# Kernel tuning notes

Hardware: AMD Instinct MI355X
Metric: run time of the kernel (lower is better)

The kernel has to match this reference:

```python
import jax, jax.numpy as jnp
import numpy as np

B, N, F, R, DEG, STEPS = 4, 1024, 128, 16, 16, 2


def setup_inputs() -> dict:
    key = jax.random.key(0)
    ks = jax.random.split(key, 12)
    BN = B * N
    E = BN * DEG

    def edges(k):
        # edges kept within each graph of size N, then offset per graph
        e = jax.random.randint(k, (2, E), 0, N)
        off = jnp.repeat(jnp.arange(B, dtype=jnp.int32) * N, N * DEG)
        return e + off[None, :]

    return {
        "x_s": jax.random.normal(ks[0], (BN, F), jnp.float32),
        "edge_index_s": edges(ks[1]),
        "x_t": jax.random.normal(ks[2], (BN, F), jnp.float32),
        "edge_index_t": edges(ks[3]),
        "W1_self": jax.random.normal(ks[4], (F, F), jnp.float32) / np.float32(np.sqrt(F)),
        "W1_nbr": jax.random.normal(ks[5], (F, F), jnp.float32) / np.float32(np.sqrt(F)),
        "b1": jnp.zeros((F,), jnp.float32),
        "W2_self": jax.random.normal(ks[6], (R, R), jnp.float32) / np.float32(np.sqrt(R)),
        "W2_nbr": jax.random.normal(ks[7], (R, R), jnp.float32) / np.float32(np.sqrt(R)),
        "b2": jnp.zeros((R,), jnp.float32),
        "Wm1": jax.random.normal(ks[8], (R, R), jnp.float32) / np.float32(np.sqrt(R)),
        "bm1": jnp.zeros((R,), jnp.float32),
        "Wm2": jax.random.normal(ks[9], (R, 1), jnp.float32) / np.float32(np.sqrt(R)),
        "bm2": jnp.zeros((1,), jnp.float32),
        "r_steps": jax.random.normal(ks[10], (STEPS, B, N, R), jnp.float32),
    }


def _psi(x, ei, Ws, Wn, b):
    # simple GraphConv: self transform + summed neighbor transform
    agg = jax.ops.segment_sum(x[ei[0]], ei[1], num_segments=x.shape[0])
    return jax.nn.relu(x @ Ws + agg @ Wn + b)


def reference(x_s, edge_index_s, x_t, edge_index_t, W1_self, W1_nbr, b1,
              W2_self, W2_nbr, b2, Wm1, bm1, Wm2, bm2, r_steps):
    # psi_1 on both graphs, then dense-batch to [B, N, F] (equal-size graphs,
    # so masks are all-True and masked_softmax == softmax)
    h_s = _psi(x_s, edge_index_s, W1_self, W1_nbr, b1).reshape(B, N, F)
    h_t = _psi(x_t, edge_index_t, W1_self, W1_nbr, b1).reshape(B, N, F)

    S_hat = jnp.einsum('bsf,btf->bst', h_s, h_t)  # [B, Ns, Nt]
    S_0 = jax.nn.softmax(S_hat, axis=-1)

    for i in range(STEPS):
        S = jax.nn.softmax(S_hat, axis=-1)
        r_s = r_steps[i]                             # [B, N, R]
        r_t = jnp.einsum('bst,bsr->btr', S, r_s)     # S^T @ r_s
        o_s = _psi(r_s.reshape(B * N, R), edge_index_s, W2_self, W2_nbr, b2).reshape(B, N, R)
        o_t = _psi(r_t.reshape(B * N, R), edge_index_t, W2_self, W2_nbr, b2).reshape(B, N, R)
        D = o_s[:, :, None, :] - o_t[:, None, :, :]  # [B, Ns, Nt, R]
        upd = (jax.nn.relu(D @ Wm1 + bm1) @ Wm2 + bm2)[..., 0]
        S_hat = S_hat + upd

    S_L = jax.nn.softmax(S_hat, axis=-1)
    return (S_0, S_L)
```

## Files before the change

### kernel.cpp

```cpp
#include <hip/hip_runtime.h>

#define B_ 4
#define N_ 1024
#define F_ 128
#define R_ 16
#define E_ 65536
#define BN_ 4096

__global__ __launch_bounds__(256) void hist_k(
    const int* __restrict__ eis, const int* __restrict__ eit, int* __restrict__ counts) {
  const int* ei = blockIdx.y ? eit : eis;
  int* c = counts + blockIdx.y * BN_;
  int e = blockIdx.x * 256 + threadIdx.x;
  atomicAdd(c + ei[E_ + e], 1);
}

__global__ __launch_bounds__(256) void csr_scan(
    const int* __restrict__ counts, int* __restrict__ offs, int* __restrict__ cursor) {
  const int* c = counts + blockIdx.x * BN_;
  int* o = offs + blockIdx.x * (BN_ + 1);
  int* cur = cursor + blockIdx.x * BN_;
  int tid = threadIdx.x;
  int base = tid * 16;
  int local[16], sum = 0;
#pragma unroll
  for (int i = 0; i < 16; i++) { local[i] = sum; sum += c[base + i]; }
  __shared__ int csum[256];
  csum[tid] = sum;
  __syncthreads();
  for (int d = 1; d < 256; d <<= 1) {
    int v = (tid >= d) ? csum[tid - d] : 0;
    __syncthreads();
    csum[tid] += v;
    __syncthreads();
  }
  int prev = (tid == 0) ? 0 : csum[tid - 1];
#pragma unroll
  for (int i = 0; i < 16; i++) { int off = prev + local[i]; o[base + i] = off; cur[base + i] = off; }
  if (tid == 255) o[BN_] = csum[255];
}

__global__ __launch_bounds__(256) void csr_fill(
    const int* __restrict__ eis, const int* __restrict__ eit,
    int* __restrict__ cursor, int* __restrict__ csr) {
  const int* ei = blockIdx.y ? eit : eis;
  int* cur = cursor + blockIdx.y * BN_;
  int* cs = csr + blockIdx.y * E_;
  int e = blockIdx.x * 256 + threadIdx.x;
  int src = ei[e], dst = ei[E_ + e];
  int pos = atomicAdd(cur + dst, 1);
  cs[pos] = src;
}

__global__ __launch_bounds__(256) void gather_f(
    const float* __restrict__ xs, const float* __restrict__ xt,
    const int* __restrict__ csr, const int* __restrict__ offs,
    float* __restrict__ aggs, float* __restrict__ aggt) {
  const float* x = blockIdx.y ? xt : xs;
  const int* cs = csr + blockIdx.y * E_;
  const int* of = offs + blockIdx.y * (BN_ + 1);
  float* agg = blockIdx.y ? aggt : aggs;
  int node = blockIdx.x * 2 + (threadIdx.x >> 7);
  int ch = threadIdx.x & 127;
  int j0 = of[node], j1 = of[node + 1];
  float a0 = 0.f, a1 = 0.f, a2 = 0.f, a3 = 0.f;
  int j = j0;
  for (; j + 3 < j1; j += 4) {
    int s0 = cs[j], s1 = cs[j + 1], s2 = cs[j + 2], s3 = cs[j + 3];
    a0 += x[(size_t)s0 * F_ + ch];
    a1 += x[(size_t)s1 * F_ + ch];
    a2 += x[(size_t)s2 * F_ + ch];
    a3 += x[(size_t)s3 * F_ + ch];
  }
  for (; j < j1; j++) a0 += x[(size_t)cs[j] * F_ + ch];
  agg[(size_t)node * F_ + ch] = (a0 + a1) + (a2 + a3);
}

__global__ __launch_bounds__(256) void psi1_gemm(
    const float* __restrict__ xs, const float* __restrict__ aggs,
    const float* __restrict__ xt, const float* __restrict__ aggt,
    const float* __restrict__ Ws, const float* __restrict__ Wn,
    const float* __restrict__ bias, float* __restrict__ hs, float* __restrict__ ht) {
  const float* x   = blockIdx.z ? xt   : xs;
  const float* agg = blockIdx.z ? aggt : aggs;
  float*       h   = blockIdx.z ? ht   : hs;
  int n0 = blockIdx.x * 64, m0 = blockIdx.y * 64;
  int tid = threadIdx.x, tx = tid & 15, ty = tid >> 4;
  __shared__ __align__(16) float sA[16][68];
  __shared__ __align__(16) float sB[16][68];
  float acc[4][4] = {};
  for (int phase = 0; phase < 2; phase++) {
    const float* A  = phase ? agg : x;
    const float* Bw = phase ? Wn  : Ws;
    for (int kb = 0; kb < F_; kb += 16) {
      int row = tid >> 2, k4 = (tid & 3) * 4;
      float4 va = *(const float4*)(A + (size_t)(m0 + row) * F_ + kb + k4);
      sA[k4 + 0][row] = va.x; sA[k4 + 1][row] = va.y;
      sA[k4 + 2][row] = va.z; sA[k4 + 3][row] = va.w;
      int k = tid >> 4, n4 = (tid & 15) * 4;
      *(float4*)&sB[k][n4] = *(const float4*)(Bw + (size_t)(kb + k) * F_ + n0 + n4);
      __syncthreads();
#pragma unroll
      for (int kk = 0; kk < 16; kk++) {
        float a[4], bb[4];
        *(float4*)a  = *(const float4*)&sA[kk][ty * 4];
        *(float4*)bb = *(const float4*)&sB[kk][tx * 4];
#pragma unroll
        for (int i = 0; i < 4; i++)
#pragma unroll
          for (int j = 0; j < 4; j++) acc[i][j] += a[i] * bb[j];
      }
      __syncthreads();
    }
  }
  float4 bv = *(const float4*)(bias + n0 + tx * 4);
  float bj[4] = {bv.x, bv.y, bv.z, bv.w};
#pragma unroll
  for (int i = 0; i < 4; i++) {
    int m = m0 + ty * 4 + i;
    float4 o;
    o.x = fmaxf(acc[i][0] + bj[0], 0.f); o.y = fmaxf(acc[i][1] + bj[1], 0.f);
    o.z = fmaxf(acc[i][2] + bj[2], 0.f); o.w = fmaxf(acc[i][3] + bj[3], 0.f);
    *(float4*)(h + (size_t)m * F_ + n0 + tx * 4) = o;
  }
}

__global__ __launch_bounds__(256) void shat_gemm(
    const float* __restrict__ hs, const float* __restrict__ ht, float* __restrict__ S) {
  int b = blockIdx.z;
  int n0 = blockIdx.x * 128, m0 = blockIdx.y * 128;
  int tid = threadIdx.x, tx = tid & 15, ty = tid >> 4;
  __shared__ __align__(16) float sA[16][132];
  __shared__ __align__(16) float sB[16][132];
  float acc[8][8] = {};
  const float* Ag = hs + (size_t)(b * N_ + m0) * F_;
  const float* Bg = ht + (size_t)(b * N_ + n0) * F_;
  for (int kb = 0; kb < F_; kb += 16) {
#pragma unroll
    for (int l = 0; l < 2; l++) {
      int idx = tid + l * 256;
      int row = idx >> 2, k4 = (idx & 3) * 4;
      float4 va = *(const float4*)(Ag + (size_t)row * F_ + kb + k4);
      sA[k4 + 0][row] = va.x; sA[k4 + 1][row] = va.y;
      sA[k4 + 2][row] = va.z; sA[k4 + 3][row] = va.w;
      float4 vb = *(const float4*)(Bg + (size_t)row * F_ + kb + k4);
      sB[k4 + 0][row] = vb.x; sB[k4 + 1][row] = vb.y;
      sB[k4 + 2][row] = vb.z; sB[k4 + 3][row] = vb.w;
    }
    __syncthreads();
#pragma unroll
    for (int kk = 0; kk < 16; kk++) {
      float a[8], bb[8];
      *(float4*)&a[0]  = *(const float4*)&sA[kk][ty * 8];
      *(float4*)&a[4]  = *(const float4*)&sA[kk][ty * 8 + 4];
      *(float4*)&bb[0] = *(const float4*)&sB[kk][tx * 8];
      *(float4*)&bb[4] = *(const float4*)&sB[kk][tx * 8 + 4];
#pragma unroll
      for (int i = 0; i < 8; i++)
#pragma unroll
        for (int j = 0; j < 8; j++) acc[i][j] += a[i] * bb[j];
    }
    __syncthreads();
  }
#pragma unroll
  for (int i = 0; i < 8; i++) {
    size_t off = ((size_t)(b * N_ + m0 + ty * 8 + i)) * N_ + n0 + tx * 8;
    float4 o0 = {acc[i][0], acc[i][1], acc[i][2], acc[i][3]};
    float4 o1 = {acc[i][4], acc[i][5], acc[i][6], acc[i][7]};
    *(float4*)(S + off) = o0; *(float4*)(S + off + 4) = o1;
  }
}

__global__ __launch_bounds__(256) void softmax_row(
    const float* __restrict__ in, float* __restrict__ out) {
  int row = blockIdx.x;
  float4 v = ((const float4*)(in + (size_t)row * N_))[threadIdx.x];
  float m = fmaxf(fmaxf(v.x, v.y), fmaxf(v.z, v.w));
#pragma unroll
  for (int o = 32; o > 0; o >>= 1) m = fmaxf(m, __shfl_down(m, o, 64));
  __shared__ float rmax[4], rsum[4];
  int wave = threadIdx.x >> 6, lane = threadIdx.x & 63;
  if (lane == 0) rmax[wave] = m;
  __syncthreads();
  m = fmaxf(fmaxf(rmax[0], rmax[1]), fmaxf(rmax[2], rmax[3]));
  float e0 = __expf(v.x - m), e1 = __expf(v.y - m);
  float e2 = __expf(v.z - m), e3 = __expf(v.w - m);
  float s = e0 + e1 + e2 + e3;
#pragma unroll
  for (int o = 32; o > 0; o >>= 1) s += __shfl_down(s, o, 64);
  if (lane == 0) rsum[wave] = s;
  __syncthreads();
  s = rsum[0] + rsum[1] + rsum[2] + rsum[3];
  float inv = 1.f / s;
  float4 o4 = {e0 * inv, e1 * inv, e2 * inv, e3 * inv};
  ((float4*)(out + (size_t)row * N_))[threadIdx.x] = o4;
}

template <bool EXP>
__global__ __launch_bounds__(256) void rt_part_k(
    const float* __restrict__ S, const float2* __restrict__ stats,
    const float* __restrict__ rs, float* __restrict__ part) {
  int b = blockIdx.z, c = blockIdx.y, t0 = blockIdx.x * 256;
  int tid = threadIdx.x;
  int s0 = c * 32;
  __shared__ float rsh[32][16];
  __shared__ float sstat[64];
  if (tid < 128) {
    int srow = tid >> 2, c4 = (tid & 3) * 4;
    float4 v = *(const float4*)(rs + ((size_t)(b * N_ + s0 + srow)) * R_ + c4);
    rsh[srow][c4] = v.x; rsh[srow][c4 + 1] = v.y;
    rsh[srow][c4 + 2] = v.z; rsh[srow][c4 + 3] = v.w;
  } else if (EXP && tid < 192) {
    sstat[tid - 128] = ((const float*)(stats + b * N_ + s0))[tid - 128];
  }
  __syncthreads();
  float acc[16] = {};
  const float* Sp = S + ((size_t)(b * N_ + s0)) * N_ + t0 + tid;
#pragma unroll
  for (int s = 0; s < 32; s++) {
    float sv = Sp[(size_t)s * N_];
    if (EXP) sv = __expf(sv - sstat[2 * s]) * sstat[2 * s + 1];
#pragma unroll
    for (int r = 0; r < 16; r++) acc[r] += sv * rsh[s][r];
  }
  float* o = part + ((size_t)((b * 32 + c) * N_) + t0 + tid) * R_;
  *(float4*)(o + 0)  = *(float4*)&acc[0];
  *(float4*)(o + 4)  = *(float4*)&acc[4];
  *(float4*)(o + 8)  = *(float4*)&acc[8];
  *(float4*)(o + 12) = *(float4*)&acc[12];
}

__global__ __launch_bounds__(256) void rt_reduce(
    const float* __restrict__ part, float* __restrict__ rt) {
  int gid = blockIdx.x * 256 + threadIdx.x;
  int b = gid >> 12, tr = gid & 4095;
  const float* p = part + (size_t)b * (32 * N_ * R_) + (size_t)tr * 4;
  float4 acc = {0.f, 0.f, 0.f, 0.f};
#pragma unroll
  for (int c = 0; c < 32; c++) {
    float4 v = *(const float4*)(p + (size_t)c * (N_ * R_));
    acc.x += v.x; acc.y += v.y; acc.z += v.z; acc.w += v.w;
  }
  ((float4*)rt)[gid] = acc;
}

__global__ __launch_bounds__(256) void gpsi2p(
    const float* __restrict__ vs, const float* __restrict__ vt,
    const int* __restrict__ csr, const int* __restrict__ offs,
    const float* __restrict__ W2s, const float* __restrict__ W2n,
    const float* __restrict__ b2, const float* __restrict__ Wm1,
    float* __restrict__ Ps, float* __restrict__ Pt4) {
  const float* v = blockIdx.y ? vt : vs;
  const int* cs = csr + blockIdx.y * E_;
  const int* of = offs + blockIdx.y * (BN_ + 1);
  int col = threadIdx.x & 15, row = threadIdx.x >> 4;
  int node = blockIdx.x * 16 + row;
  int j0 = of[node], j1 = of[node + 1];
  float a0 = 0.f, a1 = 0.f, a2 = 0.f, a3 = 0.f;
  int j = j0;
  for (; j + 3 < j1; j += 4) {
    int s0 = cs[j], s1 = cs[j + 1], s2 = cs[j + 2], s3 = cs[j + 3];
    a0 += v[(size_t)s0 * R_ + col];
    a1 += v[(size_t)s1 * R_ + col];
    a2 += v[(size_t)s2 * R_ + col];
    a3 += v[(size_t)s3 * R_ + col];
  }
  for (; j < j1; j++) a0 += v[(size_t)cs[j] * R_ + col];
  __shared__ float sWs[16][16], sWn[16][16], sWm[16][17];
  __shared__ float sv[16][17], sa[16][17], so[16][17];
  sWs[row][col] = W2s[row * 16 + col];
  sWn[row][col] = W2n[row * 16 + col];
  sWm[row][col] = Wm1[row * 16 + col];
  sv[row][col] = v[(size_t)node * R_ + col];
  sa[row][col] = (a0 + a1) + (a2 + a3);
  __syncthreads();
  float o = b2[col];
#pragma unroll
  for (int k = 0; k < 16; k++) o += sv[row][k] * sWs[k][col] + sa[row][k] * sWn[k][col];
  so[row][col] = fmaxf(o, 0.f);
  __syncthreads();
  float p = 0;
#pragma unroll
  for (int k = 0; k < 16; k++) p += so[row][k] * sWm[k][col];
  if (blockIdx.y) {
    Pt4[((size_t)(col >> 2) * BN_ + node) * 4 + (col & 3)] = p;
  } else {
    Ps[(size_t)node * R_ + col] = p;
  }
}

template <int LAST>
__device__ __forceinline__ void upd_row8_body(
    float* __restrict__ Shat, const float* __restrict__ Ps, const float* __restrict__ Pt4,
    const float* __restrict__ bm1, const float* __restrict__ Wm2,
    const float* __restrict__ bm2, float2* __restrict__ stats, float* __restrict__ SL) {
  int b = blockIdx.y, s0 = blockIdx.x * 8;
  int tid = threadIdx.x;
  int wave = tid >> 6, lane = tid & 63;
  __shared__ float ssc[8][16];
  __shared__ float sred[8][4];
  if (tid < 128) {
    int i = tid >> 4, k = tid & 15;
    ssc[i][k] = Ps[((size_t)(b * N_ + s0 + i)) * R_ + k] + bm1[k];
  }
  float swr[16];
#pragma unroll
  for (int k = 0; k < 16; k++) swr[k] = Wm2[k];
  float bm2v = bm2[0];
  __syncthreads();
  float vals[8][4];
#pragma unroll
  for (int tile = 0; tile < 4; tile++) {
    int gt = b * N_ + tile * 256 + tid;
    float pt[16];
    *(float4*)&pt[0]  = *(const float4*)(Pt4 + ((size_t)0 * BN_ + gt) * 4);
    *(float4*)&pt[4]  = *(const float4*)(Pt4 + ((size_t)1 * BN_ + gt) * 4);
    *(float4*)&pt[8]  = *(const float4*)(Pt4 + ((size_t)2 * BN_ + gt) * 4);
    *(float4*)&pt[12] = *(const float4*)(Pt4 + ((size_t)3 * BN_ + gt) * 4);
#pragma unroll
    for (int i = 0; i < 8; i++) {
      size_t rowoff = ((size_t)(b * N_ + s0 + i)) * N_ + tile * 256 + tid;
      float sh = Shat[rowoff];
      float sum = bm2v;
#pragma unroll
      for (int k = 0; k < 16; k++) sum += fmaxf(ssc[i][k] - pt[k], 0.f) * swr[k];
      float vv = sh + sum;
      vals[i][tile] = vv;
      if (!LAST) Shat[rowoff] = vv;
    }
  }
  float mrow[8], lrow[8];
#pragma unroll
  for (int i = 0; i < 8; i++) {
    float m = fmaxf(fmaxf(vals[i][0], vals[i][1]), fmaxf(vals[i][2], vals[i][3]));
#pragma unroll
    for (int o = 32; o > 0; o >>= 1) m = fmaxf(m, __shfl_down(m, o, 64));
    if (lane == 0) sred[i][wave] = m;
  }
  __syncthreads();
#pragma unroll
  for (int i = 0; i < 8; i++)
    mrow[i] = fmaxf(fmaxf(sred[i][0], sred[i][1]), fmaxf(sred[i][2], sred[i][3]));
  __syncthreads();
#pragma unroll
  for (int i = 0; i < 8; i++) {
    float e = __expf(vals[i][0] - mrow[i]) + __expf(vals[i][1] - mrow[i])
            + __expf(vals[i][2] - mrow[i]) + __expf(vals[i][3] - mrow[i]);
#pragma unroll
    for (int o = 32; o > 0; o >>= 1) e += __shfl_down(e, o, 64);
    if (lane == 0) sred[i][wave] = e;
  }
  __syncthreads();
#pragma unroll
  for (int i = 0; i < 8; i++)
    lrow[i] = (sred[i][0] + sred[i][1]) + (sred[i][2] + sred[i][3]);
  if (!LAST) {
#pragma unroll
    for (int i = 0; i < 8; i++)
      if (tid == i) stats[b * N_ + s0 + i] = make_float2(mrow[i], 1.f / lrow[i]);
  } else {
#pragma unroll
    for (int i = 0; i < 8; i++) {
      float inv = 1.f / lrow[i];
      size_t rowoff = ((size_t)(b * N_ + s0 + i)) * N_;
#pragma unroll
      for (int tile = 0; tile < 4; tile++)
        SL[rowoff + tile * 256 + tid] = __expf(vals[i][tile] - mrow[i]) * inv;
    }
  }
}

__global__ __launch_bounds__(256) void upd_row8_0(
    float* __restrict__ Shat, const float* __restrict__ Ps, const float* __restrict__ Pt4,
    const float* __restrict__ bm1, const float* __restrict__ Wm2,
    const float* __restrict__ bm2, float2* __restrict__ stats) {
  upd_row8_body<0>(Shat, Ps, Pt4, bm1, Wm2, bm2, stats, nullptr);
}

__global__ __launch_bounds__(256) void upd_row8_1(
    float* __restrict__ Shat, const float* __restrict__ Ps, const float* __restrict__ Pt4,
    const float* __restrict__ bm1, const float* __restrict__ Wm2,
    const float* __restrict__ bm2, float* __restrict__ SL) {
  upd_row8_body<1>(Shat, Ps, Pt4, bm1, Wm2, bm2, nullptr, SL);
}

extern "C" void kernel_launch(void* const* d_in, const int* in_sizes, int n_in,
                              void* d_out, int out_size, void* d_ws, size_t ws_size,
                              hipStream_t stream) {
  const float* x_s = (const float*)d_in[0];
  const int*   ei_s = (const int*)d_in[1];
  const float* x_t = (const float*)d_in[2];
  const int*   ei_t = (const int*)d_in[3];
  const float* W1s = (const float*)d_in[4];
  const float* W1n = (const float*)d_in[5];
  const float* b1  = (const float*)d_in[6];
  const float* W2s = (const float*)d_in[7];
  const float* W2n = (const float*)d_in[8];
  const float* b2  = (const float*)d_in[9];
  const float* Wm1 = (const float*)d_in[10];
  const float* bm1 = (const float*)d_in[11];
  const float* Wm2 = (const float*)d_in[12];
  const float* bm2 = (const float*)d_in[13];
  const float* r_steps = (const float*)d_in[14];

  float* out = (float*)d_out;
  float* S0 = out;
  float* SL = out + (size_t)B_ * N_ * N_;

  float* ws = (float*)d_ws;
  float* agg_s = ws;
  float* agg_t = ws + 524288;
  float* h_s   = ws + 1048576;
  float* h_t   = ws + 1572864;
  float* part  = ws;
  float* Shat  = ws + 2097152;
  float* rtb   = ws + 6291456;
  float2* stats = (float2*)(ws + 6356992);
  float* Ps    = ws + 6488064;
  float* Pt4   = ws + 6553600;
  int* counts  = (int*)(ws + 6619136);
  int* cursor  = (int*)(ws + 6627328);
  int* offs    = (int*)(ws + 6635520);
  int* csr     = (int*)(ws + 6643720);

  hipMemsetAsync(counts, 0, 2 * BN_ * sizeof(int), stream);
  hist_k<<<dim3(E_ / 256, 2), 256, 0, stream>>>(ei_s, ei_t, counts);
  csr_scan<<<2, 256, 0, stream>>>(counts, offs, cursor);
  csr_fill<<<dim3(E_ / 256, 2), 256, 0, stream>>>(ei_s, ei_t, cursor, csr);

  gather_f<<<dim3(BN_ / 2, 2), 256, 0, stream>>>(x_s, x_t, csr, offs, agg_s, agg_t);
  psi1_gemm<<<dim3(2, 64, 2), 256, 0, stream>>>(x_s, agg_s, x_t, agg_t, W1s, W1n, b1, h_s, h_t);

  shat_gemm<<<dim3(8, 8, 4), 256, 0, stream>>>(h_s, h_t, Shat);
  softmax_row<<<B_ * N_, 256, 0, stream>>>(Shat, S0);

  const float* rs0 = r_steps;
  rt_part_k<false><<<dim3(4, 32, 4), 256, 0, stream>>>(S0, nullptr, rs0, part);
  rt_reduce<<<64, 256, 0, stream>>>(part, rtb);
  gpsi2p<<<dim3(256, 2), 256, 0, stream>>>(rs0, rtb, csr, offs, W2s, W2n, b2, Wm1, Ps, Pt4);
  upd_row8_0<<<dim3(N_ / 8, B_), 256, 0, stream>>>(Shat, Ps, Pt4, bm1, Wm2, bm2, stats);

  const float* rs1 = r_steps + (size_t)B_ * N_ * R_;
  rt_part_k<true><<<dim3(4, 32, 4), 256, 0, stream>>>(Shat, stats, rs1, part);
  rt_reduce<<<64, 256, 0, stream>>>(part, rtb);
  gpsi2p<<<dim3(256, 2), 256, 0, stream>>>(rs1, rtb, csr, offs, W2s, W2n, b2, Wm1, Ps, Pt4);
  upd_row8_1<<<dim3(N_ / 8, B_), 256, 0, stream>>>(Shat, Ps, Pt4, bm1, Wm2, bm2, SL);
}
```

Measured before the change: 229.9 us.

## Fuse CSR histogram into scan, hoist source-side psi2, replace r_t reduction with atomics

The edge histogram and prefix scan now run in one kernel that counts in shared memory, which removes the memset and one launch. Source-side psi2 projections for both steps depend only on r_steps, so they are computed up front in a merged prep kernel with the feature gather and the zeroing of the r_t buffers. The partial-sum buffer and reduce kernel for r_t are replaced by float atomicAdds into a zeroed buffer, removing a launch and a large intermediate write and read. The cost is atomic contention, non-deterministic summation order, and a single-block-per-graph histogram that serialises 64K shared-memory atomics.

```diff
diff --git a/kernel.cpp b/kernel.cpp
--- a/kernel.cpp
+++ b/kernel.cpp
@@ -7,25 +7,23 @@
 #define E_ 65536
 #define BN_ 4096
 
-__global__ __launch_bounds__(256) void hist_k(
-    const int* __restrict__ eis, const int* __restrict__ eit, int* __restrict__ counts) {
-  const int* ei = blockIdx.y ? eit : eis;
-  int* c = counts + blockIdx.y * BN_;
-  int e = blockIdx.x * 256 + threadIdx.x;
-  atomicAdd(c + ei[E_ + e], 1);
-}
-
-__global__ __launch_bounds__(256) void csr_scan(
-    const int* __restrict__ counts, int* __restrict__ offs, int* __restrict__ cursor) {
-  const int* c = counts + blockIdx.x * BN_;
+__global__ __launch_bounds__(256) void histscan(
+    const int* __restrict__ eis, const int* __restrict__ eit,
+    int* __restrict__ offs, int* __restrict__ cursor) {
+  const int* ei = blockIdx.x ? eit : eis;
   int* o = offs + blockIdx.x * (BN_ + 1);
   int* cur = cursor + blockIdx.x * BN_;
   int tid = threadIdx.x;
+  __shared__ int cnt[BN_];
+  __shared__ int csum[256];
+  for (int i = tid; i < BN_; i += 256) cnt[i] = 0;
+  __syncthreads();
+  for (int e = tid; e < E_; e += 256) atomicAdd(&cnt[ei[E_ + e]], 1);
+  __syncthreads();
   int base = tid * 16;
   int local[16], sum = 0;
 #pragma unroll
-  for (int i = 0; i < 16; i++) { local[i] = sum; sum += c[base + i]; }
-  __shared__ int csum[256];
+  for (int i = 0; i < 16; i++) { local[i] = sum; sum += cnt[base + i]; }
   csum[tid] = sum;
   __syncthreads();
   for (int d = 1; d < 256; d <<= 1) {
@@ -52,28 +50,79 @@
   cs[pos] = src;
 }
 
-__global__ __launch_bounds__(256) void gather_f(
+__global__ __launch_bounds__(256) void prep2(
     const float* __restrict__ xs, const float* __restrict__ xt,
+    const float* __restrict__ r0, const float* __restrict__ r1,
     const int* __restrict__ csr, const int* __restrict__ offs,
-    float* __restrict__ aggs, float* __restrict__ aggt) {
-  const float* x = blockIdx.y ? xt : xs;
-  const int* cs = csr + blockIdx.y * E_;
-  const int* of = offs + blockIdx.y * (BN_ + 1);
-  float* agg = blockIdx.y ? aggt : aggs;
-  int node = blockIdx.x * 2 + (threadIdx.x >> 7);
-  int ch = threadIdx.x & 127;
-  int j0 = of[node], j1 = of[node + 1];
-  float a0 = 0.f, a1 = 0.f, a2 = 0.f, a3 = 0.f;
-  int j = j0;
-  for (; j + 3 < j1; j += 4) {
-    int s0 = cs[j], s1 = cs[j + 1], s2 = cs[j + 2], s3 = cs[j + 3];
-    a0 += x[(size_t)s0 * F_ + ch];
-    a1 += x[(size_t)s1 * F_ + ch];
-    a2 += x[(size_t)s2 * F_ + ch];
-    a3 += x[(size_t)s3 * F_ + ch];
-  }
-  for (; j < j1; j++) a0 += x[(size_t)cs[j] * F_ + ch];
-  agg[(size_t)node * F_ + ch] = (a0 + a1) + (a2 + a3);
+    const float* __restrict__ W2s, const float* __restrict__ W2n,
+    const float* __restrict__ b2, const float* __restrict__ Wm1,
+    float* __restrict__ aggs, float* __restrict__ aggt,
+    float* __restrict__ Ps0, float* __restrict__ Ps1,
+    float* __restrict__ rtb0, float* __restrict__ rtb1) {
+  int bid = blockIdx.x, tid = threadIdx.x;
+  __shared__ float sWs[16][16], sWn[16][16], sWm[16][17];
+  __shared__ float sv[16][17], sa[16][17], so[16][17];
+  if (bid < 4096) {
+    int side = bid >> 11, nblk = bid & 2047;
+    const float* x = side ? xt : xs;
+    float* agg = side ? aggt : aggs;
+    const int* cs = csr + side * E_;
+    const int* of = offs + side * (BN_ + 1);
+    int node = nblk * 2 + (tid >> 7);
+    int ch = tid & 127;
+    int j0 = of[node], j1 = of[node + 1];
+    float a0 = 0.f, a1 = 0.f, a2 = 0.f, a3 = 0.f;
+    int j = j0;
+    for (; j + 3 < j1; j += 4) {
+      int s0 = cs[j], s1 = cs[j + 1], s2 = cs[j + 2], s3 = cs[j + 3];
+      a0 += x[(size_t)s0 * F_ + ch];
+      a1 += x[(size_t)s1 * F_ + ch];
+      a2 += x[(size_t)s2 * F_ + ch];
+      a3 += x[(size_t)s3 * F_ + ch];
+    }
+    for (; j < j1; j++) a0 += x[(size_t)cs[j] * F_ + ch];
+    agg[(size_t)node * F_ + ch] = (a0 + a1) + (a2 + a3);
+  } else if (bid < 4608) {
+    int step = (bid >= 4352);
+    int nblk = bid - (step ? 4352 : 4096);
+    const float* v = step ? r1 : r0;
+    float* Ps = step ? Ps1 : Ps0;
+    const int* cs = csr;
+    const int* of = offs;
+    int col = tid & 15, row = tid >> 4;
+    int node = nblk * 16 + row;
+    int j0 = of[node], j1 = of[node + 1];
+    float a0 = 0.f, a1 = 0.f, a2 = 0.f, a3 = 0.f;
+    int j = j0;
+    for (; j + 3 < j1; j += 4) {
+      int s0 = cs[j], s1 = cs[j + 1], s2 = cs[j + 2], s3 = cs[j + 3];
+      a0 += v[(size_t)s0 * R_ + col];
+      a1 += v[(size_t)s1 * R_ + col];
+      a2 += v[(size_t)s2 * R_ + col];
+      a3 += v[(size_t)s3 * R_ + col];
+    }
+    for (; j < j1; j++) a0 += v[(size_t)cs[j] * R_ + col];
+    sWs[row][col] = W2s[row * 16 + col];
+    sWn[row][col] = W2n[row * 16 + col];
+    sWm[row][col] = Wm1[row * 16 + col];
+    sv[row][col] = v[(size_t)node * R_ + col];
+    sa[row][col] = (a0 + a1) + (a2 + a3);
+    __syncthreads();
+    float o = b2[col];
+#pragma unroll
+    for (int k = 0; k < 16; k++) o += sv[row][k] * sWs[k][col] + sa[row][k] * sWn[k][col];
+    so[row][col] = fmaxf(o, 0.f);
+    __syncthreads();
+    float p = 0;
+#pragma unroll
+    for (int k = 0; k < 16; k++) p += so[row][k] * sWm[k][col];
+    Ps[(size_t)node * R_ + col] = p;
+  } else {
+    int idx = (bid - 4608) * 256 + tid;
+    float4 z = {0.f, 0.f, 0.f, 0.f};
+    if (idx < 16384) ((float4*)rtb0)[idx] = z;
+    else             ((float4*)rtb1)[idx - 16384] = z;
+  }
 }
 
 __global__ __launch_bounds__(256) void psi1_gemm(
@@ -197,9 +246,9 @@
 }
 
 template <bool EXP>
-__global__ __launch_bounds__(256) void rt_part_k(
+__global__ __launch_bounds__(256) void rtscat(
     const float* __restrict__ S, const float2* __restrict__ stats,
-    const float* __restrict__ rs, float* __restrict__ part) {
+    const float* __restrict__ rs, float* __restrict__ rtb) {
   int b = blockIdx.z, c = blockIdx.y, t0 = blockIdx.x * 256;
   int tid = threadIdx.x;
   int s0 = c * 32;
@@ -223,36 +272,20 @@
 #pragma unroll
     for (int r = 0; r < 16; r++) acc[r] += sv * rsh[s][r];
   }
-  float* o = part + ((size_t)((b * 32 + c) * N_) + t0 + tid) * R_;
-  *(float4*)(o + 0)  = *(float4*)&acc[0];
-  *(float4*)(o + 4)  = *(float4*)&acc[4];
-  *(float4*)(o + 8)  = *(float4*)&acc[8];
-  *(float4*)(o + 12) = *(float4*)&acc[12];
-}
-
-__global__ __launch_bounds__(256) void rt_reduce(
-    const float* __restrict__ part, float* __restrict__ rt) {
-  int gid = blockIdx.x * 256 + threadIdx.x;
-  int b = gid >> 12, tr = gid & 4095;
-  const float* p = part + (size_t)b * (32 * N_ * R_) + (size_t)tr * 4;
-  float4 acc = {0.f, 0.f, 0.f, 0.f};
-#pragma unroll
-  for (int c = 0; c < 32; c++) {
-    float4 v = *(const float4*)(p + (size_t)c * (N_ * R_));
-    acc.x += v.x; acc.y += v.y; acc.z += v.z; acc.w += v.w;
-  }
-  ((float4*)rt)[gid] = acc;
-}
-
-__global__ __launch_bounds__(256) void gpsi2p(
-    const float* __restrict__ vs, const float* __restrict__ vt,
+  float* o = rtb + ((size_t)(b * N_) + t0 + tid) * R_;
+#pragma unroll
+  for (int r = 0; r < 16; r++) atomicAdd(o + r, acc[r]);
+}
+
+__global__ __launch_bounds__(256) void gpt(
+    const float* __restrict__ vt,
     const int* __restrict__ csr, const int* __restrict__ offs,
     const float* __restrict__ W2s, const float* __restrict__ W2n,
     const float* __restrict__ b2, const float* __restrict__ Wm1,
-    float* __restrict__ Ps, float* __restrict__ Pt4) {
-  const float* v = blockIdx.y ? vt : vs;
-  const int* cs = csr + blockIdx.y * E_;
-  const int* of = offs + blockIdx.y * (BN_ + 1);
+    float* __restrict__ Pt4) {
+  const float* v = vt;
+  const int* cs = csr + E_;
+  const int* of = offs + (BN_ + 1);
   int col = threadIdx.x & 15, row = threadIdx.x >> 4;
   int node = blockIdx.x * 16 + row;
   int j0 = of[node], j1 = of[node + 1];
@@ -282,11 +315,7 @@
   float p = 0;
 #pragma unroll
   for (int k = 0; k < 16; k++) p += so[row][k] * sWm[k][col];
-  if (blockIdx.y) {
-    Pt4[((size_t)(col >> 2) * BN_ + node) * 4 + (col & 3)] = p;
-  } else {
-    Ps[(size_t)node * R_ + col] = p;
-  }
+  Pt4[((size_t)(col >> 2) * BN_ + node) * 4 + (col & 3)] = p;
 }
 
 template <int LAST>
@@ -412,37 +441,36 @@
   float* agg_t = ws + 524288;
   float* h_s   = ws + 1048576;
   float* h_t   = ws + 1572864;
-  float* part  = ws;
   float* Shat  = ws + 2097152;
-  float* rtb   = ws + 6291456;
+  float* rtb0  = ws + 6291456;
   float2* stats = (float2*)(ws + 6356992);
-  float* Ps    = ws + 6488064;
+  float* Ps0   = ws + 6488064;
   float* Pt4   = ws + 6553600;
-  int* counts  = (int*)(ws + 6619136);
   int* cursor  = (int*)(ws + 6627328);
   int* offs    = (int*)(ws + 6635520);
   int* csr     = (int*)(ws + 6643720);
-
-  hipMemsetAsync(counts, 0, 2 * BN_ * sizeof(int), stream);
-  hist_k<<<dim3(E_ / 256, 2), 256, 0, stream>>>(ei_s, ei_t, counts);
-  csr_scan<<<2, 256, 0, stream>>>(counts, offs, cursor);
+  float* rtb1  = ws + 6774792;
+  float* Ps1   = ws + 6840328;
+
+  const float* rs0 = r_steps;
+  const float* rs1 = r_steps + (size_t)B_ * N_ * R_;
+
+  histscan<<<2, 256, 0, stream>>>(ei_s, ei_t, offs, cursor);
   csr_fill<<<dim3(E_ / 256, 2), 256, 0, stream>>>(ei_s, ei_t, cursor, csr);
 
-  gather_f<<<dim3(BN_ / 2, 2), 256, 0, stream>>>(x_s, x_t, csr, offs, agg_s, agg_t);
+  prep2<<<4736, 256, 0, stream>>>(x_s, x_t, rs0, rs1, csr, offs,
+                                  W2s, W2n, b2, Wm1,
+                                  agg_s, agg_t, Ps0, Ps1, rtb0, rtb1);
   psi1_gemm<<<dim3(2, 64, 2), 256, 0, stream>>>(x_s, agg_s, x_t, agg_t, W1s, W1n, b1, h_s, h_t);
 
   shat_gemm<<<dim3(8, 8, 4), 256, 0, stream>>>(h_s, h_t, Shat);
   softmax_row<<<B_ * N_, 256, 0, stream>>>(Shat, S0);
 
-  const float* rs0 = r_steps;
-  rt_part_k<false><<<dim3(4, 32, 4), 256, 0, stream>>>(S0, nullptr, rs0, part);
-  rt_reduce<<<64, 256, 0, stream>>>(part, rtb);
-  gpsi2p<<<dim3(256, 2), 256, 0, stream>>>(rs0, rtb, csr, offs, W2s, W2n, b2, Wm1, Ps, Pt4);
-  upd_row8_0<<<dim3(N_ / 8, B_), 256, 0, stream>>>(Shat, Ps, Pt4, bm1, Wm2, bm2, stats);
-
-  const float* rs1 = r_steps + (size_t)B_ * N_ * R_;
-  rt_part_k<true><<<dim3(4, 32, 4), 256, 0, stream>>>(Shat, stats, rs1, part);
-  rt_reduce<<<64, 256, 0, stream>>>(part, rtb);
-  gpsi2p<<<dim3(256, 2), 256, 0, stream>>>(rs1, rtb, csr, offs, W2s, W2n, b2, Wm1, Ps, Pt4);
-  upd_row8_1<<<dim3(N_ / 8, B_), 256, 0, stream>>>(Shat, Ps, Pt4, bm1, Wm2, bm2, SL);
-}
+  rtscat<false><<<dim3(4, 32, 4), 256, 0, stream>>>(S0, nullptr, rs0, rtb0);
+  gpt<<<256, 256, 0, stream>>>(rtb0, csr, offs, W2s, W2n, b2, Wm1, Pt4);
+  upd_row8_0<<<dim3(N_ / 8, B_), 256, 0, stream>>>(Shat, Ps0, Pt4, bm1, Wm2, bm2, stats);
+
+  rtscat<true><<<dim3(4, 32, 4), 256, 0, stream>>>(Shat, stats, rs1, rtb1);
+  gpt<<<256, 256, 0, stream>>>(rtb1, csr, offs, W2s, W2n, b2, Wm1, Pt4);
+  upd_row8_1<<<dim3(N_ / 8, B_), 256, 0, stream>>>(Shat, Ps1, Pt4, bm1, Wm2, bm2, SL);
+}
```

Result: slower. 525.7 us (+128.7%).

## Compute S_hat with split-bf16 MFMA instead of fp32 SIMT GEMM

Applied to the files above, without the earlier changes.

psi1_gemm now writes its outputs as hi/lo bf16 pairs, and the S_hat batched GEMM is rewritten to use bf16 16x16x32 MFMA instructions with three products (hi*hi, hi*lo, lo*hi) to approximate fp32 accuracy. The aim is to replace the slow fp32 FMA loop with matrix cores and halve the memory read for h. It gives up some precision (the lo*lo term is dropped) and the new kernel loads operands straight from global memory without LDS staging, with scattered scalar stores to S.

```diff
diff --git a/kernel.cpp b/kernel.cpp
--- a/kernel.cpp
+++ b/kernel.cpp
@@ -6,6 +6,18 @@
 #define R_ 16
 #define E_ 65536
 #define BN_ 4096
+
+typedef __attribute__((ext_vector_type(8))) short bf16x8;
+typedef __attribute__((ext_vector_type(4))) float f32x4;
+
+__device__ __forceinline__ ushort bf16_rn(float v) {
+  unsigned u = __float_as_uint(v);
+  unsigned r = u + 0x7FFFu + ((u >> 16) & 1u);
+  return (ushort)(r >> 16);
+}
+__device__ __forceinline__ float bf16_to_f(ushort h) {
+  return __uint_as_float(((unsigned)h) << 16);
+}
 
 __global__ __launch_bounds__(256) void hist_k(
     const int* __restrict__ eis, const int* __restrict__ eit, int* __restrict__ counts) {
@@ -80,10 +92,13 @@
     const float* __restrict__ xs, const float* __restrict__ aggs,
     const float* __restrict__ xt, const float* __restrict__ aggt,
     const float* __restrict__ Ws, const float* __restrict__ Wn,
-    const float* __restrict__ bias, float* __restrict__ hs, float* __restrict__ ht) {
+    const float* __restrict__ bias,
+    ushort* __restrict__ hhis, ushort* __restrict__ hlos,
+    ushort* __restrict__ hhit, ushort* __restrict__ hlot) {
   const float* x   = blockIdx.z ? xt   : xs;
   const float* agg = blockIdx.z ? aggt : aggs;
-  float*       h   = blockIdx.z ? ht   : hs;
+  ushort*      hhi = blockIdx.z ? hhit : hhis;
+  ushort*      hlo = blockIdx.z ? hlot : hlos;
   int n0 = blockIdx.x * 64, m0 = blockIdx.y * 64;
   int tid = threadIdx.x, tx = tid & 15, ty = tid >> 4;
   __shared__ __align__(16) float sA[16][68];
@@ -118,57 +133,55 @@
 #pragma unroll
   for (int i = 0; i < 4; i++) {
     int m = m0 + ty * 4 + i;
-    float4 o;
-    o.x = fmaxf(acc[i][0] + bj[0], 0.f); o.y = fmaxf(acc[i][1] + bj[1], 0.f);
-    o.z = fmaxf(acc[i][2] + bj[2], 0.f); o.w = fmaxf(acc[i][3] + bj[3], 0.f);
-    *(float4*)(h + (size_t)m * F_ + n0 + tx * 4) = o;
-  }
-}
-
-__global__ __launch_bounds__(256) void shat_gemm(
-    const float* __restrict__ hs, const float* __restrict__ ht, float* __restrict__ S) {
+    float v[4];
+#pragma unroll
+    for (int j = 0; j < 4; j++) v[j] = fmaxf(acc[i][j] + bj[j], 0.f);
+    ushort hi[4], lo[4];
+#pragma unroll
+    for (int j = 0; j < 4; j++) {
+      hi[j] = bf16_rn(v[j]);
+      lo[j] = bf16_rn(v[j] - bf16_to_f(hi[j]));
+    }
+    size_t off = (size_t)m * F_ + n0 + tx * 4;
+    *(ushort4*)(hhi + off) = make_ushort4(hi[0], hi[1], hi[2], hi[3]);
+    *(ushort4*)(hlo + off) = make_ushort4(lo[0], lo[1], lo[2], lo[3]);
+  }
+}
+
+__global__ __launch_bounds__(256) void shat_mfma(
+    const ushort* __restrict__ ahi, const ushort* __restrict__ alo,
+    const ushort* __restrict__ bhi, const ushort* __restrict__ blo,
+    float* __restrict__ S) {
   int b = blockIdx.z;
-  int n0 = blockIdx.x * 128, m0 = blockIdx.y * 128;
-  int tid = threadIdx.x, tx = tid & 15, ty = tid >> 4;
-  __shared__ __align__(16) float sA[16][132];
-  __shared__ __align__(16) float sB[16][132];
-  float acc[8][8] = {};
-  const float* Ag = hs + (size_t)(b * N_ + m0) * F_;
-  const float* Bg = ht + (size_t)(b * N_ + n0) * F_;
-  for (int kb = 0; kb < F_; kb += 16) {
-#pragma unroll
-    for (int l = 0; l < 2; l++) {
-      int idx = tid + l * 256;
-      int row = idx >> 2, k4 = (idx & 3) * 4;
-      float4 va = *(const float4*)(Ag + (size_t)row * F_ + kb + k4);
-      sA[k4 + 0][row] = va.x; sA[k4 + 1][row] = va.y;
-      sA[k4 + 2][row] = va.z; sA[k4 + 3][row] = va.w;
-      float4 vb = *(const float4*)(Bg + (size_t)row * F_ + kb + k4);
-      sB[k4 + 0][row] = vb.x; sB[k4 + 1][row] = vb.y;
-      sB[k4 + 2][row] = vb.z; sB[k4 + 3][row] = vb.w;
-    }
-    __syncthreads();
-#pragma unroll
-    for (int kk = 0; kk < 16; kk++) {
-      float a[8], bb[8];
-      *(float4*)&a[0]  = *(const float4*)&sA[kk][ty * 8];
-      *(float4*)&a[4]  = *(const float4*)&sA[kk][ty * 8 + 4];
-      *(float4*)&bb[0] = *(const float4*)&sB[kk][tx * 8];
-      *(float4*)&bb[4] = *(const float4*)&sB[kk][tx * 8 + 4];
-#pragma unroll
-      for (int i = 0; i < 8; i++)
-#pragma unroll
-        for (int j = 0; j < 8; j++) acc[i][j] += a[i] * bb[j];
-    }
-    __syncthreads();
-  }
-#pragma unroll
-  for (int i = 0; i < 8; i++) {
-    size_t off = ((size_t)(b * N_ + m0 + ty * 8 + i)) * N_ + n0 + tx * 8;
-    float4 o0 = {acc[i][0], acc[i][1], acc[i][2], acc[i][3]};
-    float4 o1 = {acc[i][4], acc[i][5], acc[i][6], acc[i][7]};
-    *(float4*)(S + off) = o0; *(float4*)(S + off + 4) = o1;
-  }
+  int n0 = blockIdx.x * 64, m0 = blockIdx.y * 64;
+  int wave = threadIdx.x >> 6, lane = threadIdx.x & 63;
+  int lr = lane & 15, kg = (lane >> 4) * 8;
+  const ushort* Ah = ahi + ((size_t)(b * N_ + m0 + wave * 16 + lr)) * F_ + kg;
+  const ushort* Al = alo + ((size_t)(b * N_ + m0 + wave * 16 + lr)) * F_ + kg;
+  const ushort* Bh = bhi + ((size_t)(b * N_ + n0 + lr)) * F_ + kg;
+  const ushort* Bl = blo + ((size_t)(b * N_ + n0 + lr)) * F_ + kg;
+  f32x4 acc[4] = {};
+#pragma unroll
+  for (int ks = 0; ks < F_; ks += 32) {
+    bf16x8 av  = *(const bf16x8*)(Ah + ks);
+    bf16x8 av2 = *(const bf16x8*)(Al + ks);
+#pragma unroll
+    for (int c = 0; c < 4; c++) {
+      bf16x8 bv  = *(const bf16x8*)(Bh + (size_t)(c * 16) * F_ + ks);
+      bf16x8 bv2 = *(const bf16x8*)(Bl + (size_t)(c * 16) * F_ + ks);
+      acc[c] = __builtin_amdgcn_mfma_f32_16x16x32_bf16(av,  bv,  acc[c], 0, 0, 0);
+      acc[c] = __builtin_amdgcn_mfma_f32_16x16x32_bf16(av,  bv2, acc[c], 0, 0, 0);
+      acc[c] = __builtin_amdgcn_mfma_f32_16x16x32_bf16(av2, bv,  acc[c], 0, 0, 0);
+    }
+  }
+#pragma unroll
+  for (int c = 0; c < 4; c++)
+#pragma unroll
+    for (int r = 0; r < 4; r++) {
+      int orow = m0 + wave * 16 + (lane >> 4) * 4 + r;
+      int ocol = n0 + c * 16 + lr;
+      S[((size_t)(b * N_ + orow)) * N_ + ocol] = acc[c][r];
+    }
 }
 
 __global__ __launch_bounds__(256) void softmax_row(
@@ -410,8 +423,10 @@
   float* ws = (float*)d_ws;
   float* agg_s = ws;
   float* agg_t = ws + 524288;
-  float* h_s   = ws + 1048576;
-  float* h_t   = ws + 1572864;
+  ushort* hhi_s = (ushort*)(ws + 1048576);
+  ushort* hlo_s = (ushort*)(ws + 1310720);
+  ushort* hhi_t = (ushort*)(ws + 1572864);
+  ushort* hlo_t = (ushort*)(ws + 1835008);
   float* part  = ws;
   float* Shat  = ws + 2097152;
   float* rtb   = ws + 6291456;
@@ -429,9 +444,10 @@
   csr_fill<<<dim3(E_ / 256, 2), 256, 0, stream>>>(ei_s, ei_t, cursor, csr);
 
   gather_f<<<dim3(BN_ / 2, 2), 256, 0, stream>>>(x_s, x_t, csr, offs, agg_s, agg_t);
-  psi1_gemm<<<dim3(2, 64, 2), 256, 0, stream>>>(x_s, agg_s, x_t, agg_t, W1s, W1n, b1, h_s, h_t);
-
-  shat_gemm<<<dim3(8, 8, 4), 256, 0, stream>>>(h_s, h_t, Shat);
+  psi1_gemm<<<dim3(2, 64, 2), 256, 0, stream>>>(x_s, agg_s, x_t, agg_t, W1s, W1n, b1,
+                                                hhi_s, hlo_s, hhi_t, hlo_t);
+
+  shat_mfma<<<dim3(16, 16, 4), 256, 0, stream>>>(hhi_s, hlo_s, hhi_t, hlo_t, Shat);
   softmax_row<<<B_ * N_, 256, 0, stream>>>(Shat, S0);
 
   const float* rs0 = r_steps;
```

Result: no change. 230.2 us (+0.1%).
